# Kernel optimization log

Measured on AMD Instinct MI355X. Metric: run time of the kernel, lower is better.

The kernel has to match this reference:

```python
import jax, jax.numpy as jnp
import numpy as np

N_NODES = 10000
N_EDGES = 160000
K = 3  # Chebyshev filter order
DIMS = [(782, 16), (16, 32), (32, 64), (64, 128), (128, 19)]


def _cheb_norm(edge_index, num_nodes):
    # PyG ChebConv norm with normalization='sym', lambda_max=2.0:
    # scaled Laplacian L_hat = 2L/lambda_max - I = -D^{-1/2} A D^{-1/2} (off-diag), diag = 0
    src, dst = edge_index[0], edge_index[1]
    w = jnp.ones(src.shape, dtype=jnp.float32)
    deg = jax.ops.segment_sum(w, src, num_segments=num_nodes)
    dinv = jnp.where(deg > 0, 1.0 / jnp.sqrt(deg), 0.0)  # masked_fill(inf) -> 0
    return -dinv[src] * dinv[dst]


def _spmm(norm, src, dst, x, num_nodes):
    # out[i] = sum_{e: dst[e]==i} norm[e] * x[src[e]]
    return jax.ops.segment_sum(norm[:, None] * x[src], dst, num_segments=num_nodes)


def _cheb_conv(x, src, dst, norm, W, b):
    # W: [K, Fin, Fout]; Chebyshev recursion T0=x, T1=L_hat x, Tk=2 L_hat T_{k-1} - T_{k-2}
    n = x.shape[0]
    Tx0 = x
    out = Tx0 @ W[0]
    Tx1 = _spmm(norm, src, dst, Tx0, n)
    out = out + Tx1 @ W[1]
    for k in range(2, W.shape[0]):
        Tx2 = 2.0 * _spmm(norm, src, dst, Tx1, n) - Tx0
        out = out + Tx2 @ W[k]
        Tx0, Tx1 = Tx1, Tx2
    return out + b


def setup_inputs() -> dict:
    key = jax.random.key(0)
    ks = jax.random.split(key, 2 + len(DIMS))
    x = jax.random.normal(ks[0], (N_NODES, 782), dtype=jnp.float32)
    edge_index = jax.random.randint(ks[1], (2, N_EDGES), 0, N_NODES)
    inp = {"x": x, "edge_index": edge_index}
    for i, (fi, fo) in enumerate(DIMS):
        inp[f"W{i+1}"] = jax.random.normal(ks[2 + i], (K, fi, fo), dtype=jnp.float32) / np.float32(np.sqrt(fi * K))
        inp[f"b{i+1}"] = jnp.zeros((fo,), dtype=jnp.float32)
    return inp


def reference(x, edge_index, W1, b1, W2, b2, W3, b3, W4, b4, W5, b5):
    src, dst = edge_index[0], edge_index[1]
    norm = _cheb_norm(edge_index, x.shape[0])
    h = jax.nn.relu(_cheb_conv(x, src, dst, norm, W1, b1))
    h = jax.nn.relu(_cheb_conv(h, src, dst, norm, W2, b2))
    h = jax.nn.relu(_cheb_conv(h, src, dst, norm, W3, b3))
    h = jax.nn.relu(_cheb_conv(h, src, dst, norm, W4, b4))
    h = _cheb_conv(h, src, dst, norm, W5, b5)
    return jax.nn.softmax(h, axis=-1)
```

## Files before the change

kernel.cpp:

```cpp
#include <hip/hip_runtime.h>
#include <math.h>

#define NN 10000
#define NE 160000
#define CAP 128
#define NT 256
#define WC1_TOTAL (782 * 48)
#define WC5_TOTAL (128 * 60)
#define L1_SPLITS 12
#define L1_KCHUNK 66
#define CNT_BLKS 625

struct MegaParams {
  const float* x;
  const int* src;
  const int* dst;
  const float* W1; const float* b1;
  const float* W2; const float* b2;
  const float* W3; const float* b3;
  const float* W4; const float* b4;
  const float* W5; const float* b5;
  int* deg; int* cnt; int* bsrc;
  float* dinv; float* wc1; float* wc5;
  float* ABC1; float* E1; float* B2; float* B3; float* B4;
  float* H4; float* ABC5; float* E5; float* P;
  float* out;
};

__device__ __forceinline__ void wcat_one(const float* __restrict__ W,
                                         float* __restrict__ Wc,
                                         int i, int Fin, int F, int Fp) {
  int w3 = 3 * Fp;
  int row = i / w3;
  int c = i - row * w3;
  int sec = c / Fp;
  int f = c - sec * Fp;
  float v = 0.0f;
  if (f < F) {
    if (sec == 0)      v = W[row * F + f] - W[2 * Fin * F + row * F + f];
    else if (sec == 1) v = W[Fin * F + row * F + f];
    else               v = W[2 * Fin * F + row * F + f];
  }
  Wc[i] = v;
}

struct Row8 { float4 lo, hi; };

template <bool AL16>
__device__ __forceinline__ Row8 ld_row8(const float* __restrict__ X, int ldx,
                                        int gr, int M, int kc, int kend) {
  Row8 r;
  r.lo = make_float4(0.f, 0.f, 0.f, 0.f);
  r.hi = make_float4(0.f, 0.f, 0.f, 0.f);
  if (gr < M && kc < kend) {
    const float* xp = X + (size_t)gr * ldx + kc;
    if (kc + 8 <= kend) {
      if (AL16) {
        r.lo = ((const float4*)xp)[0];
        r.hi = ((const float4*)xp)[1];
      } else {
        float2 a = *(const float2*)xp;
        float2 b = *(const float2*)(xp + 2);
        float2 c = *(const float2*)(xp + 4);
        float2 d = *(const float2*)(xp + 6);
        r.lo = make_float4(a.x, a.y, b.x, b.y);
        r.hi = make_float4(c.x, c.y, d.x, d.y);
      }
    } else {
      int rem = kend - kc;
      r.lo.x = xp[0];
      if (rem > 1) r.lo.y = xp[1];
      if (rem > 2) r.lo.z = xp[2];
      if (rem > 3) r.lo.w = xp[3];
      if (rem > 4) r.hi.x = xp[4];
      if (rem > 5) r.hi.y = xp[5];
      if (rem > 6) r.hi.z = xp[6];
    }
  }
  return r;
}

__device__ __forceinline__ float comp8(const Row8& r, int k) {
  switch (k) {
    case 0: return r.lo.x; case 1: return r.lo.y;
    case 2: return r.lo.z; case 3: return r.lo.w;
    case 4: return r.hi.x; case 5: return r.hi.y;
    case 6: return r.hi.z; default: return r.hi.w;
  }
}

__device__ __forceinline__ float rlane(float v, int i) {
  return __int_as_float(__builtin_amdgcn_readlane(__float_as_int(v), i));
}

template <int TN, bool AL16, bool DIRECT>
__device__ void gemm_stage(const float* __restrict__ X, int ldx,
                           const float* __restrict__ W, int ldw,
                           float* __restrict__ Y, int ldy,
                           const float* __restrict__ bias, int relu,
                           int M, int Kd, int Nd, int kchunk, int nk,
                           int tile0, int tstride, float* Ws) {
  int ntR = (M + NT - 1) / NT;
  int ntC = Nd / TN;
  int ntRC = ntR * ntC;
  int ntiles = ntRC * nk;
  constexpr int W4 = TN / 4;
  for (int tile = tile0; tile < ntiles; tile += tstride) {
    int tz = tile / ntRC;
    int rm = tile - tz * ntRC;
    int tc = rm / ntR;
    int tr = rm - tc * ntR;
    int row0 = tr * NT;
    int col0 = tc * TN;
    int k0 = tz * kchunk;
    int kend = k0 + kchunk;
    if (kend > Kd) kend = Kd;
    int k8 = ((kend - k0) + 7) & ~7;
    __syncthreads();
    for (int idx = threadIdx.x; idx < k8 * W4; idx += NT) {
      int wk = idx / W4;
      int wc = (idx - wk * W4) * 4;
      float4 wv = make_float4(0.f, 0.f, 0.f, 0.f);
      if (k0 + wk < kend)
        wv = *(const float4*)(W + (size_t)(k0 + wk) * ldw + col0 + wc);
      *(float4*)(Ws + wk * TN + wc) = wv;
    }
    __syncthreads();
    float acc[TN];
#pragma unroll
    for (int c = 0; c < TN; c++) acc[c] = 0.f;
    int r = row0 + threadIdx.x;
    int nch = k8 >> 3;
    Row8 cur = ld_row8<AL16>(X, ldx, r, M, k0, kend);
    for (int ci = 0; ci < nch; ci++) {
      Row8 nxt = cur;
      if (ci + 1 < nch) nxt = ld_row8<AL16>(X, ldx, r, M, k0 + (ci + 1) * 8, kend);
      int kb = ci << 3;
#pragma unroll
      for (int k = 0; k < 8; k++) {
        float x0 = comp8(cur, k);
        const float* wr = Ws + (kb + k) * TN;
#pragma unroll
        for (int c = 0; c < TN; c += 4) {
          float4 wv = *(const float4*)(wr + c);
          acc[c + 0] += x0 * wv.x; acc[c + 1] += x0 * wv.y;
          acc[c + 2] += x0 * wv.z; acc[c + 3] += x0 * wv.w;
        }
      }
      cur = nxt;
    }
    if (r < M) {
      if (DIRECT) {
        float* yr = Y + (size_t)r * ldy + col0;
#pragma unroll
        for (int c = 0; c < TN; c += 4) {
          float4 v;
          v.x = acc[c + 0] + (bias ? bias[col0 + c + 0] : 0.f);
          v.y = acc[c + 1] + (bias ? bias[col0 + c + 1] : 0.f);
          v.z = acc[c + 2] + (bias ? bias[col0 + c + 2] : 0.f);
          v.w = acc[c + 3] + (bias ? bias[col0 + c + 3] : 0.f);
          if (relu) {
            v.x = fmaxf(v.x, 0.f); v.y = fmaxf(v.y, 0.f);
            v.z = fmaxf(v.z, 0.f); v.w = fmaxf(v.w, 0.f);
          }
          *(float4*)(yr + c) = v;
        }
      } else {
        float* pr = Y + ((size_t)tz * M + r) * Nd + col0;
#pragma unroll
        for (int c = 0; c < TN; c += 4)
          *(float4*)(pr + c) = make_float4(acc[c], acc[c + 1], acc[c + 2], acc[c + 3]);
      }
    }
  }
}

__device__ void spmm_stage(const int* __restrict__ cnt,
                           const int* __restrict__ bsrc,
                           const float* __restrict__ dinv,
                           const float* __restrict__ X, int ldx,
                           float* __restrict__ Y, int ldy,
                           const float* __restrict__ add, int lda,
                           const float* __restrict__ bias,
                           float alpha, float beta,
                           int C_log2, int Fstore, int relu, int do_softmax) {
  int wv = threadIdx.x >> 6;
  int lane = threadIdx.x & 63;
  int C = 1 << C_log2;
  int chunk = lane & (C - 1);
  int eslot = lane >> C_log2;
  int Epar = 64 >> C_log2;
  for (int node = blockIdx.x * 4 + wv; node < NN; node += gridDim.x * 4) {
    int cn = cnt[node]; if (cn > CAP) cn = CAP;
    float dn = dinv[node];
    int j0 = node << 7;
    int j1 = j0 + cn;
    float sx = 0.f, sy = 0.f, sz = 0.f, sw = 0.f;
    for (int j = j0 + eslot; j < j1; j += Epar) {
      int sn = bsrc[j];
      float w = dinv[sn];
      float4 xv = *(const float4*)(X + (size_t)sn * ldx + (chunk << 2));
      sx += w * xv.x; sy += w * xv.y; sz += w * xv.z; sw += w * xv.w;
    }
    for (int st = C; st < 64; st <<= 1) {
      sx += __shfl_xor(sx, st);
      sy += __shfl_xor(sy, st);
      sz += __shfl_xor(sz, st);
      sw += __shfl_xor(sw, st);
    }
    if (eslot == 0) {
      float am = -alpha * dn;
      int f0 = chunk << 2;
      float4 u = make_float4(am * sx, am * sy, am * sz, am * sw);
      if (add) {
        float4 av = *(const float4*)(add + (size_t)node * lda + f0);
        u.x += beta * av.x; u.y += beta * av.y; u.z += beta * av.z; u.w += beta * av.w;
      }
      if (bias) {
        if (f0 + 0 < Fstore) u.x += bias[f0 + 0];
        if (f0 + 1 < Fstore) u.y += bias[f0 + 1];
        if (f0 + 2 < Fstore) u.z += bias[f0 + 2];
        if (f0 + 3 < Fstore) u.w += bias[f0 + 3];
      }
      if (!do_softmax) {
        if (relu) {
          u.x = fmaxf(u.x, 0.f); u.y = fmaxf(u.y, 0.f);
          u.z = fmaxf(u.z, 0.f); u.w = fmaxf(u.w, 0.f);
        }
        if (f0 + 4 <= Fstore) {
          *(float4*)(Y + (size_t)node * ldy + f0) = u;
        } else {
          float vv[4] = {u.x, u.y, u.z, u.w};
#pragma unroll
          for (int c = 0; c < 4; c++)
            if (f0 + c < Fstore) Y[(size_t)node * ldy + f0 + c] = vv[c];
        }
      } else {
        float v[4] = {u.x, u.y, u.z, u.w};
        float mx = -INFINITY;
#pragma unroll
        for (int c = 0; c < 4; c++)
          if (f0 + c < Fstore) mx = fmaxf(mx, v[c]);
        mx = fmaxf(mx, __shfl_xor(mx, 1));
        mx = fmaxf(mx, __shfl_xor(mx, 2));
        mx = fmaxf(mx, __shfl_xor(mx, 4));
        float e[4];
        float s = 0.f;
#pragma unroll
        for (int c = 0; c < 4; c++) {
          e[c] = (f0 + c < Fstore) ? __expf(v[c] - mx) : 0.f;
          s += e[c];
        }
        s += __shfl_xor(s, 1);
        s += __shfl_xor(s, 2);
        s += __shfl_xor(s, 4);
        float inv = 1.f / s;
#pragma unroll
        for (int c = 0; c < 4; c++) {
          int f = f0 + c;
          if (f < Fstore) Y[(size_t)node * ldy + f] = e[c] * inv;
        }
      }
    }
  }
}

template <int F, int C_log2, int LD, int KK, int FOUT, int LDO>
__global__ __launch_bounds__(NT) void k_fused_t2gemm(
    const int* __restrict__ cnt, const int* __restrict__ bsrc,
    const float* __restrict__ dinv, const float* __restrict__ B,
    const float* __restrict__ W, const float* __restrict__ bias,
    float* __restrict__ Y) {
  int wv = threadIdx.x >> 6;
  int lane = threadIdx.x & 63;
  constexpr int C = 1 << C_log2;
  int chunk = lane & (C - 1);
  int eslot = lane >> C_log2;
  constexpr int Epar = 64 >> C_log2;
  int col = lane % FOUT;
  float wr[KK];
#pragma unroll
  for (int k = 0; k < KK; k++) wr[k] = W[k * FOUT + col];
  float bb = bias[col];
  for (int node = blockIdx.x * 4 + wv; node < NN; node += gridDim.x * 4) {
    int cn = cnt[node]; if (cn > CAP) cn = CAP;
    float dn = dinv[node];
    int j0 = node << 7, j1 = j0 + cn;
    float sx = 0.f, sy = 0.f, sz = 0.f, sw = 0.f;
    for (int j = j0 + eslot; j < j1; j += Epar) {
      int sn = bsrc[j];
      float w = dinv[sn];
      float4 xv = *(const float4*)(B + (size_t)sn * LD + F + (chunk << 2));
      sx += w * xv.x; sy += w * xv.y; sz += w * xv.z; sw += w * xv.w;
    }
#pragma unroll
    for (int st = C; st < 64; st <<= 1) {
      sx += __shfl_xor(sx, st);
      sy += __shfl_xor(sy, st);
      sz += __shfl_xor(sz, st);
      sw += __shfl_xor(sw, st);
    }
    int ridx = (lane < 2 * F) ? lane : (lane - 2 * F);
    float rv0 = B[(size_t)node * LD + ridx];
    int f = (KK == 48) ? (lane - 2 * F) : lane;
    int cc = (f >> 2) & (C - 1);
    float a0 = __shfl(sx, cc), a1 = __shfl(sy, cc);
    float a2 = __shfl(sz, cc), a3 = __shfl(sw, cc);
    int comp = f & 3;
    float Ssel = (comp == 0) ? a0 : (comp == 1) ? a1 : (comp == 2) ? a2 : a3;
    float t2v = fmaf(-2.f * dn, Ssel, -rv0);
    float acc = bb;
    if (KK == 48) {
      float rv = (lane < 2 * F) ? rv0 : t2v;
#pragma unroll
      for (int k = 0; k < 48; k++) acc = fmaf(rlane(rv, k), wr[k], acc);
    } else {
#pragma unroll
      for (int k = 0; k < 64; k++) acc = fmaf(rlane(rv0, k), wr[k], acc);
#pragma unroll
      for (int k = 64; k < 96; k++) acc = fmaf(rlane(t2v, k - 64), wr[k], acc);
    }
    acc = fmaxf(acc, 0.f);
    if (lane < FOUT) Y[(size_t)node * LDO + col] = acc;
  }
}


__global__ __launch_bounds__(NT) void k_zero_wcat(MegaParams p) {
  int tid = blockIdx.x * NT + threadIdx.x;
  int TT = gridDim.x * NT;
  for (int i = tid; i < 2 * NN; i += TT) p.deg[i] = 0;
  for (int i = tid; i < WC1_TOTAL; i += TT) wcat_one(p.W1, p.wc1, i, 782, 16, 16);
  for (int i = tid; i < WC5_TOTAL; i += TT) wcat_one(p.W5, p.wc5, i, 128, 19, 20);
}

__global__ __launch_bounds__(NT) void k_count_gemm1(MegaParams p) {
  __shared__ float Ws[72 * 48];
  if (blockIdx.x < CNT_BLKS) {
    int e = blockIdx.x * NT + threadIdx.x;
    int s = p.src[e], d = p.dst[e];
    atomicAdd(&p.deg[s], 1);
    int slot = atomicAdd(&p.cnt[d], 1);
    if (slot < CAP) p.bsrc[(d << 7) + slot] = s;
  } else {
    gemm_stage<48, false, false>(p.x, 782, p.wc1, 48, p.P, 0, nullptr, 0,
                                 NN, 782, 48, L1_KCHUNK, L1_SPLITS,
                                 blockIdx.x - CNT_BLKS, 1 << 30, Ws);
  }
}

__global__ __launch_bounds__(NT) void k_reduce_dinv(MegaParams p) {
  int tid = blockIdx.x * NT + threadIdx.x;
  int TT = gridDim.x * NT;
  for (int i = tid; i < NN; i += TT) {
    int d = p.deg[i];
    p.dinv[i] = d > 0 ? 1.0f / sqrtf((float)d) : 0.0f;
  }
  for (int i = tid; i < NN * 48; i += TT) {
    float s = 0.f;
#pragma unroll
    for (int z = 0; z < L1_SPLITS; z++) s += p.P[(size_t)z * (NN * 48) + i];
    p.ABC1[i] = s;
  }
}

__global__ __launch_bounds__(NT) void k_spmm(
    const int* cnt, const int* bsrc, const float* dinv,
    const float* X, int ldx, float* Y, int ldy,
    const float* add, int lda, const float* bias,
    float alpha, float beta, int C_log2, int Fstore, int relu, int do_softmax) {
  spmm_stage(cnt, bsrc, dinv, X, ldx, Y, ldy, add, lda, bias,
             alpha, beta, C_log2, Fstore, relu, do_softmax);
}

__global__ __launch_bounds__(NT, 2) void k_gemm16(
    const float* X, int ldx, const float* W, int ldw, float* Y, int ldy,
    const float* bias, int relu, int Kd, int Nd) {
  __shared__ float Ws[192 * 16];
  gemm_stage<16, true, true>(X, ldx, W, ldw, Y, ldy, bias, relu,
                             NN, Kd, Nd, Kd, 1, blockIdx.x, gridDim.x, Ws);
}
__global__ __launch_bounds__(NT, 2) void k_gemm20(
    const float* X, int ldx, const float* W, int ldw, float* Y, int ldy,
    const float* bias, int relu, int Kd, int Nd) {
  __shared__ float Ws[128 * 20];
  gemm_stage<20, true, true>(X, ldx, W, ldw, Y, ldy, bias, relu,
                             NN, Kd, Nd, Kd, 1, blockIdx.x, gridDim.x, Ws);
}


extern "C" void kernel_launch(void* const* d_in, const int* in_sizes, int n_in,
                              void* d_out, int out_size, void* d_ws, size_t ws_size,
                              hipStream_t stream) {
  (void)in_sizes; (void)n_in; (void)out_size; (void)ws_size;
  char* p = (char*)d_ws;
  auto alloc = [&](size_t bytes) {
    char* r = p;
    p += (bytes + 255) & ~(size_t)255;
    return r;
  };
  int*   i_deg  = (int*)alloc(sizeof(int) * NN * 2);
  int*   i_bsrc = (int*)alloc(sizeof(int) * NN * CAP);
  float* f_dinv = (float*)alloc(sizeof(float) * NN);
  float* wc1    = (float*)alloc(sizeof(float) * WC1_TOTAL);
  float* wc5    = (float*)alloc(sizeof(float) * WC5_TOTAL);
  float* R1     = (float*)alloc(sizeof(float) * NN * 96);
  float* R2     = (float*)alloc(sizeof(float) * NN * 192);
  float* R3     = (float*)alloc(sizeof(float) * NN * 128);
  float* P      = (float*)alloc(sizeof(float) * NN * 48 * L1_SPLITS);

  MegaParams mp;
  mp.x   = (const float*)d_in[0];
  const int* ei = (const int*)d_in[1];
  mp.src = ei;
  mp.dst = ei + NE;
  mp.W1 = (const float*)d_in[2];  mp.b1 = (const float*)d_in[3];
  mp.W2 = (const float*)d_in[4];  mp.b2 = (const float*)d_in[5];
  mp.W3 = (const float*)d_in[6];  mp.b3 = (const float*)d_in[7];
  mp.W4 = (const float*)d_in[8];  mp.b4 = (const float*)d_in[9];
  mp.W5 = (const float*)d_in[10]; mp.b5 = (const float*)d_in[11];
  mp.deg = i_deg; mp.cnt = i_deg + NN; mp.bsrc = i_bsrc;
  mp.dinv = f_dinv; mp.wc1 = wc1; mp.wc5 = wc5;
  mp.ABC1 = R1; mp.B3 = R1; mp.ABC5 = R1;
  mp.E1 = R2;   mp.B4 = R2; mp.E5 = R2;
  mp.B2 = R3;   mp.H4 = R3;
  mp.P = P;
  mp.out = (float*)d_out;

  k_zero_wcat<<<160, NT, 0, stream>>>(mp);
  k_count_gemm1<<<CNT_BLKS + 480, NT, 0, stream>>>(mp);
  k_reduce_dinv<<<(NN * 48 + NT - 1) / NT, NT, 0, stream>>>(mp);
  k_spmm<<<2500, NT, 0, stream>>>(mp.cnt, mp.bsrc, mp.dinv, mp.ABC1 + 32, 48,
                                  mp.E1, 16, mp.ABC1 + 16, 48, nullptr,
                                  2.f, 1.f, 2, 16, 0, 0);
  k_spmm<<<2500, NT, 0, stream>>>(mp.cnt, mp.bsrc, mp.dinv, mp.E1, 16,
                                  mp.B2, 48, mp.ABC1, 48, mp.b1,
                                  1.f, 1.f, 2, 16, 1, 0);
  k_spmm<<<2500, NT, 0, stream>>>(mp.cnt, mp.bsrc, mp.dinv, mp.B2, 48,
                                  mp.B2 + 16, 48, nullptr, 0, nullptr,
                                  1.f, 0.f, 2, 16, 0, 0);
  k_fused_t2gemm<16, 2, 48, 48, 32, 96><<<1250, NT, 0, stream>>>(
      mp.cnt, mp.bsrc, mp.dinv, mp.B2, mp.W2, mp.b2, mp.B3);
  k_spmm<<<2500, NT, 0, stream>>>(mp.cnt, mp.bsrc, mp.dinv, mp.B3, 96,
                                  mp.B3 + 32, 96, nullptr, 0, nullptr,
                                  1.f, 0.f, 3, 32, 0, 0);
  k_fused_t2gemm<32, 3, 96, 96, 64, 192><<<1250, NT, 0, stream>>>(
      mp.cnt, mp.bsrc, mp.dinv, mp.B3, mp.W3, mp.b3, mp.B4);
  k_spmm<<<2500, NT, 0, stream>>>(mp.cnt, mp.bsrc, mp.dinv, mp.B4, 192,
                                  mp.B4 + 64, 192, nullptr, 0, nullptr,
                                  1.f, 0.f, 4, 64, 0, 0);
  k_spmm<<<2500, NT, 0, stream>>>(mp.cnt, mp.bsrc, mp.dinv, mp.B4 + 64, 192,
                                  mp.B4 + 128, 192, mp.B4, 192, nullptr,
                                  2.f, -1.f, 4, 64, 0, 0);
  k_gemm16<<<320, NT, 0, stream>>>(mp.B4, 192, mp.W4, 128, mp.H4, 128, mp.b4, 1,
                                   192, 128);
  k_gemm20<<<120, NT, 0, stream>>>(mp.H4, 128, mp.wc5, 60, mp.ABC5, 60, nullptr, 0,
                                   128, 60);
  k_spmm<<<2500, NT, 0, stream>>>(mp.cnt, mp.bsrc, mp.dinv, mp.ABC5 + 40, 60,
                                  mp.E5, 32, mp.ABC5 + 20, 60, nullptr,
                                  2.f, 1.f, 3, 20, 0, 0);
  k_spmm<<<2500, NT, 0, stream>>>(mp.cnt, mp.bsrc, mp.dinv, mp.E5, 32,
                                  mp.out, 19, mp.ABC5, 60, mp.b5,
                                  1.f, 1.f, 3, 19, 0, 1);
}
```

Before: 256.2 us.

## Transpose x into a column-major buffer and use a row-per-thread layer-1 GEMM

Adds a transpose of the 10000x782 input x into a feature-major scratch buffer, done by extra blocks in the first kernel through a padded shared-memory tile. Layer 1's split-K GEMM is replaced by a kernel where each thread owns one node row, reads coalesced feature columns from the transposed buffer with register prefetch, and accumulates all 48 outputs against weights held in shared memory. This aims to make the x reads coalesced and raise arithmetic reuse. The cost is an extra full read and write of x (about 31 MB) plus a 48-float accumulator per thread, which raises register pressure.

```diff
diff --git a/kernel.cpp b/kernel.cpp
--- a/kernel.cpp
+++ b/kernel.cpp
@@ -10,6 +10,7 @@
 #define L1_SPLITS 12
 #define L1_KCHUNK 66
 #define CNT_BLKS 625
+#define TRP_BLKS (157 * 13)
 
 struct MegaParams {
   const float* x;
@@ -24,6 +25,7 @@
   float* dinv; float* wc1; float* wc5;
   float* ABC1; float* E1; float* B2; float* B3; float* B4;
   float* H4; float* ABC5; float* E5; float* P;
+  float* XT;
   float* out;
 };
 
@@ -175,6 +177,74 @@
   }
 }
 
+__device__ void gemm1_xt(const float* __restrict__ XT,
+                         const float* __restrict__ Wf,
+                         float* __restrict__ P,
+                         int tile, float* Ws) {
+  const int ntR = 40;
+  int tz = tile / ntR;
+  int tr = tile - tz * ntR;
+  int row0 = tr * NT;
+  int k0 = tz * L1_KCHUNK;
+  int kend = k0 + L1_KCHUNK;
+  if (kend > 782) kend = 782;
+  int k8 = ((kend - k0) + 7) & ~7;
+  for (int idx = threadIdx.x; idx < k8 * 12; idx += NT) {
+    int wk = idx / 12;
+    int wc = (idx - wk * 12) * 4;
+    float4 wv = make_float4(0.f, 0.f, 0.f, 0.f);
+    if (k0 + wk < kend)
+      wv = *(const float4*)(Wf + (size_t)(k0 + wk) * 48 + wc);
+    *(float4*)(Ws + wk * 48 + wc) = wv;
+  }
+  __syncthreads();
+  float acc[48];
+#pragma unroll
+  for (int c = 0; c < 48; c++) acc[c] = 0.f;
+  int r = row0 + threadIdx.x;
+  bool rv = r < NN;
+  int nch = k8 >> 3;
+  float cur[8];
+#pragma unroll
+  for (int j = 0; j < 8; j++) {
+    int kk = k0 + j;
+    cur[j] = (rv && kk < kend) ? XT[(size_t)kk * NN + r] : 0.f;
+  }
+  for (int ci = 0; ci < nch; ci++) {
+    float nxt[8];
+#pragma unroll
+    for (int j = 0; j < 8; j++) nxt[j] = cur[j];
+    if (ci + 1 < nch) {
+      int kb2 = k0 + (ci + 1) * 8;
+#pragma unroll
+      for (int j = 0; j < 8; j++) {
+        int kk = kb2 + j;
+        nxt[j] = (rv && kk < kend) ? XT[(size_t)kk * NN + r] : 0.f;
+      }
+    }
+    int kb = ci << 3;
+#pragma unroll
+    for (int k = 0; k < 8; k++) {
+      float x0 = cur[k];
+      const float* wr = Ws + (kb + k) * 48;
+#pragma unroll
+      for (int c = 0; c < 48; c += 4) {
+        float4 wv = *(const float4*)(wr + c);
+        acc[c + 0] += x0 * wv.x; acc[c + 1] += x0 * wv.y;
+        acc[c + 2] += x0 * wv.z; acc[c + 3] += x0 * wv.w;
+      }
+    }
+#pragma unroll
+    for (int j = 0; j < 8; j++) cur[j] = nxt[j];
+  }
+  if (rv) {
+    float* pr = P + ((size_t)tz * NN + r) * 48;
+#pragma unroll
+    for (int c = 0; c < 48; c += 4)
+      *(float4*)(pr + c) = make_float4(acc[c], acc[c + 1], acc[c + 2], acc[c + 3]);
+  }
+}
+
 __device__ void spmm_stage(const int* __restrict__ cnt,
                            const int* __restrict__ bsrc,
                            const float* __restrict__ dinv,
@@ -327,11 +397,31 @@
 
 
 __global__ __launch_bounds__(NT) void k_zero_wcat(MegaParams p) {
-  int tid = blockIdx.x * NT + threadIdx.x;
-  int TT = gridDim.x * NT;
-  for (int i = tid; i < 2 * NN; i += TT) p.deg[i] = 0;
-  for (int i = tid; i < WC1_TOTAL; i += TT) wcat_one(p.W1, p.wc1, i, 782, 16, 16);
-  for (int i = tid; i < WC5_TOTAL; i += TT) wcat_one(p.W5, p.wc5, i, 128, 19, 20);
+  if (blockIdx.x < 32) {
+    int tid = blockIdx.x * NT + threadIdx.x;
+    int TT = 32 * NT;
+    for (int i = tid; i < 2 * NN; i += TT) p.deg[i] = 0;
+    for (int i = tid; i < WC1_TOTAL; i += TT) wcat_one(p.W1, p.wc1, i, 782, 16, 16);
+    for (int i = tid; i < WC5_TOTAL; i += TT) wcat_one(p.W5, p.wc5, i, 128, 19, 20);
+  } else {
+    __shared__ float ts[64][65];
+    int b = blockIdx.x - 32;
+    int tr = b % 157, tc = b / 157;
+    int row0 = tr * 64, col0 = tc * 64;
+    for (int i = threadIdx.x; i < 4096; i += NT) {
+      int rr = i >> 6, cc = i & 63;
+      float v = 0.f;
+      if (row0 + rr < NN && col0 + cc < 782)
+        v = p.x[(size_t)(row0 + rr) * 782 + col0 + cc];
+      ts[rr][cc] = v;
+    }
+    __syncthreads();
+    for (int i = threadIdx.x; i < 4096; i += NT) {
+      int kk = i >> 6, rr = i & 63;
+      if (col0 + kk < 782 && row0 + rr < NN)
+        p.XT[(size_t)(col0 + kk) * NN + row0 + rr] = ts[rr][kk];
+    }
+  }
 }
 
 __global__ __launch_bounds__(NT) void k_count_gemm1(MegaParams p) {
@@ -343,9 +433,7 @@
     int slot = atomicAdd(&p.cnt[d], 1);
     if (slot < CAP) p.bsrc[(d << 7) + slot] = s;
   } else {
-    gemm_stage<48, false, false>(p.x, 782, p.wc1, 48, p.P, 0, nullptr, 0,
-                                 NN, 782, 48, L1_KCHUNK, L1_SPLITS,
-                                 blockIdx.x - CNT_BLKS, 1 << 30, Ws);
+    gemm1_xt(p.XT, p.wc1, p.P, blockIdx.x - CNT_BLKS, Ws);
   }
 }
 
@@ -408,6 +496,7 @@
   float* R2     = (float*)alloc(sizeof(float) * NN * 192);
   float* R3     = (float*)alloc(sizeof(float) * NN * 128);
   float* P      = (float*)alloc(sizeof(float) * NN * 48 * L1_SPLITS);
+  float* XT     = (float*)alloc(sizeof(float) * 782 * NN);
 
   MegaParams mp;
   mp.x   = (const float*)d_in[0];
@@ -425,9 +514,10 @@
   mp.E1 = R2;   mp.B4 = R2; mp.E5 = R2;
   mp.B2 = R3;   mp.H4 = R3;
   mp.P = P;
+  mp.XT = XT;
   mp.out = (float*)d_out;
 
-  k_zero_wcat<<<160, NT, 0, stream>>>(mp);
+  k_zero_wcat<<<32 + TRP_BLKS, NT, 0, stream>>>(mp);
   k_count_gemm1<<<CNT_BLKS + 480, NT, 0, stream>>>(mp);
   k_reduce_dinv<<<(NN * 48 + NT - 1) / NT, NT, 0, stream>>>(mp);
   k_spmm<<<2500, NT, 0, stream>>>(mp.cnt, mp.bsrc, mp.dinv, mp.ABC1 + 32, 48,
```

New measurement: 270.6 us. 5.6% more time.
